# Performance work log

Hardware: AMD Instinct MI355X
Metric: run time of the kernel (lower is better)

Reference implementation:

```python
import jax, jax.numpy as jnp
import numpy as np

DIM = 1024
HEADS = 16
DIM_HEAD = 64
INNER = HEADS * DIM_HEAD  # 1024
SCALE = DIM_HEAD ** -0.5


def setup_inputs() -> dict:
    key = jax.random.key(0)
    k0, k1, k2 = jax.random.split(key, 3)
    x = jax.random.normal(k0, (4, 2048, DIM), dtype=jnp.float32)
    ln_gamma = jnp.ones((DIM,), dtype=jnp.float32)
    ln_beta = jnp.zeros((DIM,), dtype=jnp.float32)
    w_qkv = jax.random.normal(k1, (DIM, 3 * INNER), dtype=jnp.float32) * (DIM ** -0.5)
    w_out = jax.random.normal(k2, (INNER, DIM), dtype=jnp.float32) * (INNER ** -0.5)
    b_out = jnp.zeros((DIM,), dtype=jnp.float32)
    return {"x": x, "ln_gamma": ln_gamma, "ln_beta": ln_beta,
            "w_qkv": w_qkv, "w_out": w_out, "b_out": b_out}


def reference(x, ln_gamma, ln_beta, w_qkv, w_out, b_out):
    # LayerNorm over last dim (eps matches torch default 1e-5)
    mu = jnp.mean(x, axis=-1, keepdims=True)
    var = jnp.mean(jnp.square(x - mu), axis=-1, keepdims=True)
    xn = (x - mu) * jax.lax.rsqrt(var + 1e-5) * ln_gamma + ln_beta
    # QKV projection (no bias)
    qkv = xn @ w_qkv  # [b, t, 3*inner]
    q, k, v = jnp.split(qkv, 3, axis=-1)
    B, T, _ = x.shape
    def to_heads(t):
        return t.reshape(B, T, HEADS, DIM_HEAD).transpose(0, 2, 1, 3)  # b h t d
    q, k, v = to_heads(q), to_heads(k), to_heads(v)
    dots = jnp.einsum('bhid,bhjd->bhij', q, k) * SCALE
    attn = jax.nn.softmax(dots, axis=-1)
    out = jnp.einsum('bhij,bhjd->bhid', attn, v)
    out = out.transpose(0, 2, 1, 3).reshape(B, T, INNER)
    return out @ w_out + b_out
```

## Files before the change

### kernel.cpp

```cpp
#include <hip/hip_runtime.h>


#define DIMX 1024
#define TSEQ 2048
#define NB 4
#define NH 16
#define DH 64
#define NROWS (NB * TSEQ)
#define QSCALE 0.18033688011112042f

typedef __bf16 bf16_t;
typedef __bf16 bf16x8 __attribute__((ext_vector_type(8)));
typedef __bf16 bf16x4 __attribute__((ext_vector_type(4)));
typedef float f32x4 __attribute__((ext_vector_type(4)));

#if __has_builtin(__builtin_amdgcn_exp2f)
#define EXP2F __builtin_amdgcn_exp2f
#else
#define EXP2F exp2f
#endif

__device__ __forceinline__ bf16x4 cvt4(f32x4 v) {
    return __builtin_convertvector(v, bf16x4);
}
__device__ __forceinline__ void async16(const bf16_t* g, bf16_t* l) {
    __builtin_amdgcn_global_load_lds(
        (const __attribute__((address_space(1))) unsigned int*)g,
        (__attribute__((address_space(3))) unsigned int*)l, 16, 0, 0);
}

__global__ __launch_bounds__(256) void prep_kernel(
    const float* __restrict__ x, const float* __restrict__ g,
    const float* __restrict__ b, bf16_t* __restrict__ xn,
    const float* __restrict__ w_qkv, bf16_t* __restrict__ wqkvT,
    const float* __restrict__ w_out, bf16_t* __restrict__ woutT) {
    int bid = blockIdx.x, tid = threadIdx.x;
    if (bid < NROWS) {
        int row = bid;
        const float4 xv = *(const float4*)(x + (size_t)row * DIMX + tid * 4);
        float s = xv.x + xv.y + xv.z + xv.w;
        float q = xv.x * xv.x + xv.y * xv.y + xv.z * xv.z + xv.w * xv.w;
        for (int o = 32; o > 0; o >>= 1) {
            s += __shfl_xor(s, o);
            q += __shfl_xor(q, o);
        }
        __shared__ float2 red[4];
        int wave = tid >> 6, lane = tid & 63;
        if (lane == 0) red[wave] = make_float2(s, q);
        __syncthreads();
        float2 r0 = red[0], r1 = red[1], r2 = red[2], r3 = red[3];
        s = r0.x + r1.x + r2.x + r3.x;
        q = r0.y + r1.y + r2.y + r3.y;
        float mu = s * (1.0f / DIMX);
        float var = q * (1.0f / DIMX) - mu * mu;
        float rstd = rsqrtf(var + 1e-5f);
        float4 gv = *(const float4*)(g + tid * 4);
        float4 bv = *(const float4*)(b + tid * 4);
        f32x4 r;
        r[0] = (xv.x - mu) * rstd * gv.x + bv.x;
        r[1] = (xv.y - mu) * rstd * gv.y + bv.y;
        r[2] = (xv.z - mu) * rstd * gv.z + bv.z;
        r[3] = (xv.w - mu) * rstd * gv.w + bv.w;
        *(bf16x4*)(xn + (size_t)row * DIMX + tid * 4) = cvt4(r);
    } else {
        const float* src;
        bf16_t* dst;
        int R, C, tb;
        if (bid < NROWS + 3072) {
            tb = bid - NROWS; src = w_qkv; dst = wqkvT; R = 1024; C = 3072;
        } else {
            tb = bid - NROWS - 3072; src = w_out; dst = woutT; R = 1024; C = 1024;
        }
        int ntx = C >> 5;
        int c0 = (tb % ntx) * 32, r0 = (tb / ntx) * 32;
        int tx = tid & 31, ty = tid >> 5;
        __shared__ float tile[32][33];
        for (int i = ty; i < 32; i += 8)
            tile[i][tx] = src[(size_t)(r0 + i) * C + c0 + tx];
        __syncthreads();
        for (int i = ty; i < 32; i += 8)
            dst[(size_t)(c0 + i) * R + r0 + tx] = (bf16_t)tile[tx][i];
    }
}

#define MFMA16 __builtin_amdgcn_mfma_f32_16x16x32_bf16

template <int MODE>
__global__ __launch_bounds__(256, 2) void gemm128p(
    const bf16_t* __restrict__ A, const bf16_t* __restrict__ BT,
    void* __restrict__ Cout, const float* __restrict__ bias, int M, int N, int K) {
    __shared__ __align__(16) bf16_t As[2][128 * 64];
    __shared__ __align__(16) bf16_t Bs[2][128 * 64];
    int tid = threadIdx.x, lane = tid & 63, wave = tid >> 6;
    int lm = lane & 15, quad = lane >> 4;
    int wr = wave >> 1, wc = wave & 1;

    int nbx = gridDim.x;
    int nwg = nbx * gridDim.y;
    int linear = blockIdx.y * nbx + blockIdx.x;
    int cpx = nwg >> 3;
    int swz = (linear & 7) * cpx + (linear >> 3);
    int bx = swz % nbx, by = swz / nbx;
    int m0 = by * 128, n0 = bx * 128;

    int srow = tid >> 3, sc8 = tid & 7;
    int scol = (sc8 ^ (srow & 7)) << 3;
    const bf16_t* ga = A + (size_t)(m0 + srow) * K + scol;
    const bf16_t* gb = BT + (size_t)(n0 + srow) * K + scol;
    int ldst = tid << 3;

    int sw0 = ((quad ^ (lm & 7)) << 3);
    int sw1 = (((4 + quad) ^ (lm & 7)) << 3);

    f32x4 zero = {0.f, 0.f, 0.f, 0.f};
    f32x4 acc[4][4];
#pragma unroll
    for (int i = 0; i < 4; ++i)
#pragma unroll
        for (int j = 0; j < 4; ++j) acc[i][j] = zero;

#pragma unroll
    for (int i = 0; i < 4; ++i) async16(ga + (size_t)(i * 32) * K, &As[0][i * 2048 + ldst]);
#pragma unroll
    for (int i = 0; i < 4; ++i) async16(gb + (size_t)(i * 32) * K, &Bs[0][i * 2048 + ldst]);
    asm volatile("s_waitcnt vmcnt(0)" ::: "memory");
    __builtin_amdgcn_s_barrier();

    int nkt = K >> 6;
    for (int kt = 0; kt < nkt; ++kt) {
        int c = kt & 1;
        int k1 = (kt + 1) << 6;
        bool pf = (kt + 1) < nkt;
        const bf16_t* pa = &As[c][0];
        const bf16_t* pb = &Bs[c][0];
        bf16_t* na = &As[c ^ 1][0];
        bf16_t* nb = &Bs[c ^ 1][0];
        bf16x8 af[4][2], bfr[4][2];

#pragma unroll
        for (int t = 0; t < 4; ++t) {
            int ro = (wr * 64 + t * 16 + lm) * 64;
            af[t][0] = *(const bf16x8*)&pa[ro + sw0];
            af[t][1] = *(const bf16x8*)&pa[ro + sw1];
        }
#pragma unroll
        for (int t = 0; t < 4; ++t) {
            int ro = (wc * 64 + t * 16 + lm) * 64;
            bfr[t][0] = *(const bf16x8*)&pb[ro + sw0];
            bfr[t][1] = *(const bf16x8*)&pb[ro + sw1];
        }
        if (pf) {
#pragma unroll
            for (int i = 0; i < 4; ++i)
                async16(ga + (size_t)(i * 32) * K + k1, &na[i * 2048 + ldst]);
#pragma unroll
            for (int i = 0; i < 4; ++i)
                async16(gb + (size_t)(i * 32) * K + k1, &nb[i * 2048 + ldst]);
        }
        asm volatile("s_waitcnt lgkmcnt(0)" ::: "memory");
        __builtin_amdgcn_s_setprio(1);
#pragma unroll
        for (int mt = 0; mt < 4; ++mt)
#pragma unroll
            for (int nt = 0; nt < 4; ++nt) {
                acc[mt][nt] = MFMA16(af[mt][0], bfr[nt][0], acc[mt][nt], 0, 0, 0);
                acc[mt][nt] = MFMA16(af[mt][1], bfr[nt][1], acc[mt][nt], 0, 0, 0);
            }
        __builtin_amdgcn_s_setprio(0);
        asm volatile("s_waitcnt vmcnt(0)" ::: "memory");
        __builtin_amdgcn_s_barrier();
    }

#pragma unroll
    for (int mt = 0; mt < 4; ++mt) {
#pragma unroll
        for (int nt = 0; nt < 4; ++nt) {
            int m = m0 + wr * 64 + mt * 16 + quad * 4;
            int n = n0 + wc * 64 + nt * 16 + lm;
            if (MODE == 1) {
                int sel = n >> 10, nn = n & 1023, h = nn >> 6, d = nn & 63;
                int b = m >> 11, t = m & 2047;
                if (sel == 2) {
                    *(bf16x4*)((bf16_t*)Cout + (size_t)2 * 8388608 +
                               ((size_t)((b * NH + h) * DH + d)) * TSEQ + t) = cvt4(acc[mt][nt]);
                } else {
                    f32x4 sv = acc[mt][nt] * (sel == 0 ? QSCALE : 1.0f);
                    bf16x4 c4 = cvt4(sv);
#pragma unroll
                    for (int r = 0; r < 4; ++r)
                        ((bf16_t*)Cout)[(size_t)sel * 8388608 +
                                        ((size_t)((b * NH + h) * TSEQ + t + r)) * DH + d] = c4[r];
                }
            } else {
                float bn = bias[n];
#pragma unroll
                for (int r = 0; r < 4; ++r)
                    ((float*)Cout)[(size_t)(m + r) * N + n] = acc[mt][nt][r] + bn;
            }
        }
    }
}

__global__ __launch_bounds__(512, 4) void attn_mfma(
    const bf16_t* __restrict__ qkv, bf16_t* __restrict__ o) {
    int bh = blockIdx.y;
    int qt = blockIdx.x;
    const bf16_t* qb = qkv + (size_t)bh * TSEQ * DH;
    const bf16_t* kb = qkv + (size_t)8388608 + (size_t)bh * TSEQ * DH;
    const bf16_t* vb = qkv + (size_t)16777216 + (size_t)bh * DH * TSEQ;
    int tid = threadIdx.x, wave = tid >> 6, lane = tid & 63;
    int lm = lane & 15, quad = lane >> 4, lx = lm & 7;

    __shared__ __align__(16) bf16_t Ks[2][2][64 * 64];
    __shared__ __align__(16) bf16_t Vt[2][2][64 * 64];

    int roff = tid >> 3;
    int fr = (roff & 3) | ((roff & 8) >> 1);
    int cperm = ((tid & 7) ^ fr) * 8;
    const bf16_t* kp = kb + (size_t)roff * DH + cperm;
    const bf16_t* vp = vb + (size_t)roff * TSEQ + cperm;
    int l0 = tid * 8;

    bf16x8 qf[2][2];
#pragma unroll
    for (int u = 0; u < 2; ++u)
#pragma unroll
        for (int ks = 0; ks < 2; ++ks)
            qf[u][ks] = *(const bf16x8*)(qb +
                (size_t)(qt * 256 + wave * 32 + u * 16 + lm) * DH + ks * 32 + quad * 8);

    f32x4 zero = {0.f, 0.f, 0.f, 0.f};
    f32x4 m16 = {-16.f, -16.f, -16.f, -16.f};
    f32x4 acc[2][4];
#pragma unroll
    for (int u = 0; u < 2; ++u)
#pragma unroll
        for (int dt = 0; dt < 4; ++dt) acc[u][dt] = zero;
    f32x4 l4[2] = {zero, zero};

    int qh = lm >> 2, rr = lm & 3;
    int krow0 = 8 * qh + rr;
    int krow1 = krow0 + 4;
    int krow2 = 32 + 8 * (qh ^ 2) + rr;
    int krow3 = krow2 + 4;
    int fo0 = (quad ^ lx) * 8;
    int fo1 = ((4 + quad) ^ lx) * 8;
    int fv = (lm & 3) | ((lm & 8) >> 1);
    int vo0 = (quad ^ fv) * 8;
    int vo1 = ((4 | (quad ^ 2)) ^ fv) * 8;

    async16(kp, &Ks[0][0][l0]);
    async16(kp + (size_t)64 * DH, &Ks[0][1][l0]);
    async16(vp, &Vt[0][0][l0]);
    async16(vp + 64, &Vt[0][1][l0]);
    kp += 128 * DH; vp += 128;
    asm volatile("s_waitcnt vmcnt(0)" ::: "memory");
    __builtin_amdgcn_s_barrier();

    for (int jt = 0; jt < TSEQ / 128; ++jt) {
        int c = jt & 1;
        if (jt + 1 < TSEQ / 128) {
            async16(kp, &Ks[c ^ 1][0][l0]);
            async16(kp + (size_t)64 * DH, &Ks[c ^ 1][1][l0]);
            async16(vp, &Vt[c ^ 1][0][l0]);
            async16(vp + 64, &Vt[c ^ 1][1][l0]);
            kp += 128 * DH; vp += 128;
        }

#pragma unroll
        for (int sub = 0; sub < 2; ++sub) {
            const bf16_t* Kc = &Ks[c][sub][0];
            const bf16_t* Vc = &Vt[c][sub][0];

            bf16x8 kf[4][2];
            kf[0][0] = *(const bf16x8*)&Kc[krow0 * 64 + fo0];
            kf[0][1] = *(const bf16x8*)&Kc[krow0 * 64 + fo1];
            kf[1][0] = *(const bf16x8*)&Kc[krow1 * 64 + fo0];
            kf[1][1] = *(const bf16x8*)&Kc[krow1 * 64 + fo1];
            kf[2][0] = *(const bf16x8*)&Kc[krow2 * 64 + fo0];
            kf[2][1] = *(const bf16x8*)&Kc[krow2 * 64 + fo1];
            kf[3][0] = *(const bf16x8*)&Kc[krow3 * 64 + fo0];
            kf[3][1] = *(const bf16x8*)&Kc[krow3 * 64 + fo1];

            bf16x8 pf[2][2];
#pragma unroll
            for (int u = 0; u < 2; ++u) {
                f32x4 s[4];
                __builtin_amdgcn_s_setprio(1);
#pragma unroll
                for (int nt = 0; nt < 4; ++nt) {
                    s[nt] = __builtin_amdgcn_mfma_f32_16x16x32_bf16(kf[nt][0], qf[u][0], m16, 0, 0, 0);
                    s[nt] = __builtin_amdgcn_mfma_f32_16x16x32_bf16(kf[nt][1], qf[u][1], s[nt], 0, 0, 0);
                }
                __builtin_amdgcn_s_setprio(0);
                f32x4 p[4];
#pragma unroll
                for (int nt = 0; nt < 4; ++nt) {
#pragma unroll
                    for (int e = 0; e < 4; ++e) p[nt][e] = EXP2F(s[nt][e]);
                    l4[u] += p[nt];
                }
                bf16x4 c0 = cvt4(p[0]), c1 = cvt4(p[1]), c2 = cvt4(p[2]), c3 = cvt4(p[3]);
                pf[u][0] = __builtin_shufflevector(c0, c1, 0, 1, 2, 3, 4, 5, 6, 7);
                pf[u][1] = __builtin_shufflevector(c2, c3, 0, 1, 2, 3, 4, 5, 6, 7);
            }

            __builtin_amdgcn_s_setprio(1);
#pragma unroll
            for (int dt = 0; dt < 4; ++dt) {
                bf16x8 vf0 = *(const bf16x8*)&Vc[(dt * 16 + lm) * 64 + vo0];
                bf16x8 vf1 = *(const bf16x8*)&Vc[(dt * 16 + lm) * 64 + vo1];
#pragma unroll
                for (int u = 0; u < 2; ++u) {
                    acc[u][dt] = __builtin_amdgcn_mfma_f32_16x16x32_bf16(vf0, pf[u][0], acc[u][dt], 0, 0, 0);
                    acc[u][dt] = __builtin_amdgcn_mfma_f32_16x16x32_bf16(vf1, pf[u][1], acc[u][dt], 0, 0, 0);
                }
            }
            __builtin_amdgcn_s_setprio(0);
        }

        asm volatile("s_waitcnt vmcnt(0)" ::: "memory");
        __builtin_amdgcn_s_barrier();
    }

    int b = bh >> 4, h = bh & 15;
#pragma unroll
    for (int u = 0; u < 2; ++u) {
        float l = (l4[u][0] + l4[u][1]) + (l4[u][2] + l4[u][3]);
        l += __shfl_xor(l, 16);
        l += __shfl_xor(l, 32);
        float rl = 1.0f / l;
        int t = qt * 256 + wave * 32 + u * 16 + lm;
#pragma unroll
        for (int dt = 0; dt < 4; ++dt) {
            f32x4 ov = acc[u][dt] * rl;
            *(bf16x4*)(o + ((size_t)(b * TSEQ + t)) * DIMX + h * DH + dt * 16 + quad * 4) = cvt4(ov);
        }
    }
}

extern "C" void kernel_launch(void* const* d_in, const int* in_sizes, int n_in,
                              void* d_out, int out_size, void* d_ws, size_t ws_size,
                              hipStream_t stream) {
    const float* x = (const float*)d_in[0];
    const float* g = (const float*)d_in[1];
    const float* be = (const float*)d_in[2];
    const float* w_qkv = (const float*)d_in[3];
    const float* w_out = (const float*)d_in[4];
    const float* b_out = (const float*)d_in[5];
    float* out = (float*)d_out;
    char* ws = (char*)d_ws;

    bf16_t* xn = (bf16_t*)(ws);
    bf16_t* wqkvT = (bf16_t*)(ws + 16777216);
    bf16_t* woutT = (bf16_t*)(ws + 23068672);
    bf16_t* qkv = (bf16_t*)(ws + 25165824);
    bf16_t* attno = (bf16_t*)(ws + 75497472);

    prep_kernel<<<NROWS + 3072 + 1024, 256, 0, stream>>>(
        x, g, be, xn, w_qkv, wqkvT, w_out, woutT);
    gemm128p<1><<<dim3(24, 64), 256, 0, stream>>>(xn, wqkvT, (void*)qkv, nullptr, NROWS, 3072, 1024);
    attn_mfma<<<dim3(8, 64), 512, 0, stream>>>(qkv, attno);
    gemm128p<2><<<dim3(8, 64), 256, 0, stream>>>(attno, woutT, (void*)out, b_out, NROWS, 1024, 1024);
}
```

Before: 261.9 us.

## Add BK=32 GEMM for QKV projection and split B-fragment loads in out-proj GEMM

Adds a new GEMM kernel, used for the QKV projection, with a 32-wide K tile. This halves shared memory per block so 4 blocks can be resident per CU instead of 2, aiming to hide latency through higher occupancy at the cost of twice as many barrier-synchronised k-iterations. The output-projection GEMM is restructured to load B fragments in two halves with extra barriers, cutting register pressure but adding synchronisation. The shared epilogue is factored into a helper function.

```diff
diff --git a/kernel.cpp b/kernel.cpp
--- a/kernel.cpp
+++ b/kernel.cpp
@@ -86,91 +86,9 @@
 #define MFMA16 __builtin_amdgcn_mfma_f32_16x16x32_bf16
 
 template <int MODE>
-__global__ __launch_bounds__(256, 2) void gemm128p(
-    const bf16_t* __restrict__ A, const bf16_t* __restrict__ BT,
-    void* __restrict__ Cout, const float* __restrict__ bias, int M, int N, int K) {
-    __shared__ __align__(16) bf16_t As[2][128 * 64];
-    __shared__ __align__(16) bf16_t Bs[2][128 * 64];
-    int tid = threadIdx.x, lane = tid & 63, wave = tid >> 6;
-    int lm = lane & 15, quad = lane >> 4;
-    int wr = wave >> 1, wc = wave & 1;
-
-    int nbx = gridDim.x;
-    int nwg = nbx * gridDim.y;
-    int linear = blockIdx.y * nbx + blockIdx.x;
-    int cpx = nwg >> 3;
-    int swz = (linear & 7) * cpx + (linear >> 3);
-    int bx = swz % nbx, by = swz / nbx;
-    int m0 = by * 128, n0 = bx * 128;
-
-    int srow = tid >> 3, sc8 = tid & 7;
-    int scol = (sc8 ^ (srow & 7)) << 3;
-    const bf16_t* ga = A + (size_t)(m0 + srow) * K + scol;
-    const bf16_t* gb = BT + (size_t)(n0 + srow) * K + scol;
-    int ldst = tid << 3;
-
-    int sw0 = ((quad ^ (lm & 7)) << 3);
-    int sw1 = (((4 + quad) ^ (lm & 7)) << 3);
-
-    f32x4 zero = {0.f, 0.f, 0.f, 0.f};
-    f32x4 acc[4][4];
-#pragma unroll
-    for (int i = 0; i < 4; ++i)
-#pragma unroll
-        for (int j = 0; j < 4; ++j) acc[i][j] = zero;
-
-#pragma unroll
-    for (int i = 0; i < 4; ++i) async16(ga + (size_t)(i * 32) * K, &As[0][i * 2048 + ldst]);
-#pragma unroll
-    for (int i = 0; i < 4; ++i) async16(gb + (size_t)(i * 32) * K, &Bs[0][i * 2048 + ldst]);
-    asm volatile("s_waitcnt vmcnt(0)" ::: "memory");
-    __builtin_amdgcn_s_barrier();
-
-    int nkt = K >> 6;
-    for (int kt = 0; kt < nkt; ++kt) {
-        int c = kt & 1;
-        int k1 = (kt + 1) << 6;
-        bool pf = (kt + 1) < nkt;
-        const bf16_t* pa = &As[c][0];
-        const bf16_t* pb = &Bs[c][0];
-        bf16_t* na = &As[c ^ 1][0];
-        bf16_t* nb = &Bs[c ^ 1][0];
-        bf16x8 af[4][2], bfr[4][2];
-
-#pragma unroll
-        for (int t = 0; t < 4; ++t) {
-            int ro = (wr * 64 + t * 16 + lm) * 64;
-            af[t][0] = *(const bf16x8*)&pa[ro + sw0];
-            af[t][1] = *(const bf16x8*)&pa[ro + sw1];
-        }
-#pragma unroll
-        for (int t = 0; t < 4; ++t) {
-            int ro = (wc * 64 + t * 16 + lm) * 64;
-            bfr[t][0] = *(const bf16x8*)&pb[ro + sw0];
-            bfr[t][1] = *(const bf16x8*)&pb[ro + sw1];
-        }
-        if (pf) {
-#pragma unroll
-            for (int i = 0; i < 4; ++i)
-                async16(ga + (size_t)(i * 32) * K + k1, &na[i * 2048 + ldst]);
-#pragma unroll
-            for (int i = 0; i < 4; ++i)
-                async16(gb + (size_t)(i * 32) * K + k1, &nb[i * 2048 + ldst]);
-        }
-        asm volatile("s_waitcnt lgkmcnt(0)" ::: "memory");
-        __builtin_amdgcn_s_setprio(1);
-#pragma unroll
-        for (int mt = 0; mt < 4; ++mt)
-#pragma unroll
-            for (int nt = 0; nt < 4; ++nt) {
-                acc[mt][nt] = MFMA16(af[mt][0], bfr[nt][0], acc[mt][nt], 0, 0, 0);
-                acc[mt][nt] = MFMA16(af[mt][1], bfr[nt][1], acc[mt][nt], 0, 0, 0);
-            }
-        __builtin_amdgcn_s_setprio(0);
-        asm volatile("s_waitcnt vmcnt(0)" ::: "memory");
-        __builtin_amdgcn_s_barrier();
-    }
-
+__device__ __forceinline__ void gemm_epilogue(
+    f32x4 (&acc)[4][4], void* Cout, const float* bias,
+    int m0, int n0, int wr, int wc, int lm, int quad, int N) {
 #pragma unroll
     for (int mt = 0; mt < 4; ++mt) {
 #pragma unroll
@@ -201,6 +119,192 @@
     }
 }
 
+template <int MODE>
+__global__ __launch_bounds__(256, 4) void gemm128s(
+    const bf16_t* __restrict__ A, const bf16_t* __restrict__ BT,
+    void* __restrict__ Cout, const float* __restrict__ bias, int M, int N, int K) {
+    __shared__ __align__(16) bf16_t As[2][128 * 32];
+    __shared__ __align__(16) bf16_t Bs[2][128 * 32];
+    int tid = threadIdx.x, lane = tid & 63, wave = tid >> 6;
+    int lm = lane & 15, quad = lane >> 4;
+    int wr = wave >> 1, wc = wave & 1;
+
+    int nbx = gridDim.x;
+    int nwg = nbx * gridDim.y;
+    int linear = blockIdx.y * nbx + blockIdx.x;
+    int cpx = nwg >> 3;
+    int swz = (linear & 7) * cpx + (linear >> 3);
+    int bx = swz % nbx, by = swz / nbx;
+    int m0 = by * 128, n0 = bx * 128;
+
+    int srow = tid >> 2;
+    int scol = ((tid & 3) ^ ((tid >> 3) & 3)) << 3;
+    const bf16_t* ga = A + (size_t)(m0 + srow) * K + scol;
+    const bf16_t* gb = BT + (size_t)(n0 + srow) * K + scol;
+    int ldst = tid * 8;
+
+    int swr = ((quad ^ ((lm >> 1) & 3)) << 3);
+
+    f32x4 zero = {0.f, 0.f, 0.f, 0.f};
+    f32x4 acc[4][4];
+#pragma unroll
+    for (int i = 0; i < 4; ++i)
+#pragma unroll
+        for (int j = 0; j < 4; ++j) acc[i][j] = zero;
+
+    async16(ga, &As[0][ldst]);
+    async16(ga + (size_t)64 * K, &As[0][2048 + ldst]);
+    async16(gb, &Bs[0][ldst]);
+    async16(gb + (size_t)64 * K, &Bs[0][2048 + ldst]);
+    asm volatile("s_waitcnt vmcnt(0)" ::: "memory");
+    __builtin_amdgcn_s_barrier();
+
+    int nkt = K >> 5;
+    for (int kt = 0; kt < nkt; ++kt) {
+        int c = kt & 1;
+        int k1 = (kt + 1) << 5;
+        bool pf = (kt + 1) < nkt;
+        const bf16_t* pa = &As[c][0];
+        const bf16_t* pb = &Bs[c][0];
+        bf16_t* na = &As[c ^ 1][0];
+        bf16_t* nb = &Bs[c ^ 1][0];
+        bf16x8 af[4], bfr[4];
+#pragma unroll
+        for (int t = 0; t < 4; ++t)
+            af[t] = *(const bf16x8*)&pa[(wr * 64 + t * 16 + lm) * 32 + swr];
+#pragma unroll
+        for (int t = 0; t < 4; ++t)
+            bfr[t] = *(const bf16x8*)&pb[(wc * 64 + t * 16 + lm) * 32 + swr];
+        if (pf) {
+            async16(ga + k1, &na[ldst]);
+            async16(ga + (size_t)64 * K + k1, &na[2048 + ldst]);
+            async16(gb + k1, &nb[ldst]);
+            async16(gb + (size_t)64 * K + k1, &nb[2048 + ldst]);
+        }
+        asm volatile("s_waitcnt lgkmcnt(0)" ::: "memory");
+        __builtin_amdgcn_s_setprio(1);
+#pragma unroll
+        for (int mt = 0; mt < 4; ++mt)
+#pragma unroll
+            for (int nt = 0; nt < 4; ++nt)
+                acc[mt][nt] = MFMA16(af[mt], bfr[nt], acc[mt][nt], 0, 0, 0);
+        __builtin_amdgcn_s_setprio(0);
+        asm volatile("s_waitcnt vmcnt(0)" ::: "memory");
+        __builtin_amdgcn_s_barrier();
+    }
+
+    gemm_epilogue<MODE>(acc, Cout, bias, m0, n0, wr, wc, lm, quad, N);
+}
+
+template <int MODE>
+__global__ __launch_bounds__(256, 2) void gemm128p(
+    const bf16_t* __restrict__ A, const bf16_t* __restrict__ BT,
+    void* __restrict__ Cout, const float* __restrict__ bias, int M, int N, int K) {
+    __shared__ __align__(16) bf16_t As[2][128 * 64];
+    __shared__ __align__(16) bf16_t Bs[2][128 * 64];
+    int tid = threadIdx.x, lane = tid & 63, wave = tid >> 6;
+    int lm = lane & 15, quad = lane >> 4;
+    int wr = wave >> 1, wc = wave & 1;
+
+    int nbx = gridDim.x;
+    int nwg = nbx * gridDim.y;
+    int linear = blockIdx.y * nbx + blockIdx.x;
+    int cpx = nwg >> 3;
+    int swz = (linear & 7) * cpx + (linear >> 3);
+    int bx = swz % nbx, by = swz / nbx;
+    int m0 = by * 128, n0 = bx * 128;
+
+    int srow = tid >> 3, sc8 = tid & 7;
+    int scol = (sc8 ^ (srow & 7)) << 3;
+    const bf16_t* ga = A + (size_t)(m0 + srow) * K + scol;
+    const bf16_t* gb = BT + (size_t)(n0 + srow) * K + scol;
+    int ldst = tid << 3;
+
+    int sw0 = ((quad ^ (lm & 7)) << 3);
+    int sw1 = (((4 + quad) ^ (lm & 7)) << 3);
+
+    f32x4 zero = {0.f, 0.f, 0.f, 0.f};
+    f32x4 acc[4][4];
+#pragma unroll
+    for (int i = 0; i < 4; ++i)
+#pragma unroll
+        for (int j = 0; j < 4; ++j) acc[i][j] = zero;
+
+#pragma unroll
+    for (int i = 0; i < 4; ++i) async16(ga + (size_t)(i * 32) * K, &As[0][i * 2048 + ldst]);
+#pragma unroll
+    for (int i = 0; i < 4; ++i) async16(gb + (size_t)(i * 32) * K, &Bs[0][i * 2048 + ldst]);
+    asm volatile("s_waitcnt vmcnt(0)" ::: "memory");
+    __builtin_amdgcn_s_barrier();
+
+    int nkt = K >> 6;
+    for (int kt = 0; kt < nkt; ++kt) {
+        int c = kt & 1;
+        int k1 = (kt + 1) << 6;
+        bool pf = (kt + 1) < nkt;
+        const bf16_t* pa = &As[c][0];
+        const bf16_t* pb = &Bs[c][0];
+        bf16_t* na = &As[c ^ 1][0];
+        bf16_t* nb = &Bs[c ^ 1][0];
+        bf16x8 af[4][2], bfr[2][2];
+
+#pragma unroll
+        for (int t = 0; t < 4; ++t) {
+            int ro = (wr * 64 + t * 16 + lm) * 64;
+            af[t][0] = *(const bf16x8*)&pa[ro + sw0];
+            af[t][1] = *(const bf16x8*)&pa[ro + sw1];
+        }
+#pragma unroll
+        for (int t = 0; t < 2; ++t) {
+            int ro = (wc * 64 + t * 16 + lm) * 64;
+            bfr[t][0] = *(const bf16x8*)&pb[ro + sw0];
+            bfr[t][1] = *(const bf16x8*)&pb[ro + sw1];
+        }
+        if (pf) {
+#pragma unroll
+            for (int i = 0; i < 4; ++i)
+                async16(ga + (size_t)(i * 32) * K + k1, &na[i * 2048 + ldst]);
+#pragma unroll
+            for (int i = 0; i < 4; ++i)
+                async16(gb + (size_t)(i * 32) * K + k1, &nb[i * 2048 + ldst]);
+        }
+        __builtin_amdgcn_s_barrier();
+        asm volatile("s_waitcnt lgkmcnt(0)" ::: "memory");
+        __builtin_amdgcn_s_setprio(1);
+#pragma unroll
+        for (int mt = 0; mt < 4; ++mt)
+#pragma unroll
+            for (int nt = 0; nt < 2; ++nt) {
+                acc[mt][nt] = MFMA16(af[mt][0], bfr[nt][0], acc[mt][nt], 0, 0, 0);
+                acc[mt][nt] = MFMA16(af[mt][1], bfr[nt][1], acc[mt][nt], 0, 0, 0);
+            }
+        __builtin_amdgcn_s_setprio(0);
+        __builtin_amdgcn_s_barrier();
+
+#pragma unroll
+        for (int t = 0; t < 2; ++t) {
+            int ro = (wc * 64 + (2 + t) * 16 + lm) * 64;
+            bfr[t][0] = *(const bf16x8*)&pb[ro + sw0];
+            bfr[t][1] = *(const bf16x8*)&pb[ro + sw1];
+        }
+        __builtin_amdgcn_s_barrier();
+        asm volatile("s_waitcnt lgkmcnt(0)" ::: "memory");
+        __builtin_amdgcn_s_setprio(1);
+#pragma unroll
+        for (int mt = 0; mt < 4; ++mt)
+#pragma unroll
+            for (int nt = 0; nt < 2; ++nt) {
+                acc[mt][2 + nt] = MFMA16(af[mt][0], bfr[nt][0], acc[mt][2 + nt], 0, 0, 0);
+                acc[mt][2 + nt] = MFMA16(af[mt][1], bfr[nt][1], acc[mt][2 + nt], 0, 0, 0);
+            }
+        __builtin_amdgcn_s_setprio(0);
+        asm volatile("s_waitcnt vmcnt(0)" ::: "memory");
+        __builtin_amdgcn_s_barrier();
+    }
+
+    gemm_epilogue<MODE>(acc, Cout, bias, m0, n0, wr, wc, lm, quad, N);
+}
+
 __global__ __launch_bounds__(512, 4) void attn_mfma(
     const bf16_t* __restrict__ qkv, bf16_t* __restrict__ o) {
     int bh = blockIdx.y;
@@ -359,7 +463,7 @@
 
     prep_kernel<<<NROWS + 3072 + 1024, 256, 0, stream>>>(
         x, g, be, xn, w_qkv, wqkvT, w_out, woutT);
-    gemm128p<1><<<dim3(24, 64), 256, 0, stream>>>(xn, wqkvT, (void*)qkv, nullptr, NROWS, 3072, 1024);
+    gemm128s<1><<<dim3(24, 64), 256, 0, stream>>>(xn, wqkvT, (void*)qkv, nullptr, NROWS, 3072, 1024);
     attn_mfma<<<dim3(8, 64), 512, 0, stream>>>(qkv, attno);
     gemm128p<2><<<dim3(8, 64), 256, 0, stream>>>(attno, woutT, (void*)out, b_out, NROWS, 1024, 1024);
 }
```

After: 268.0 us. +2.3%, slower.

## Replace double-buffered GEMM with 4-stage K=32 async pipeline

Applied to the files above, without the earlier changes.

The GEMM kernel now uses a 4-deep ring of K=32 shared-memory tiles instead of two K=64 buffers. Three tiles are prefetched ahead, with partial vmcnt waits so global loads overlap several MFMA iterations. The goal is to hide global memory latency better at the same LDS footprint. In exchange, each barrier covers half as much MFMA work, so barriers and LDS read rounds double, and the swizzle pattern changes for the 32-wide rows.

```diff
diff --git a/kernel.cpp b/kernel.cpp
--- a/kernel.cpp
+++ b/kernel.cpp
@@ -86,91 +86,9 @@
 #define MFMA16 __builtin_amdgcn_mfma_f32_16x16x32_bf16
 
 template <int MODE>
-__global__ __launch_bounds__(256, 2) void gemm128p(
-    const bf16_t* __restrict__ A, const bf16_t* __restrict__ BT,
-    void* __restrict__ Cout, const float* __restrict__ bias, int M, int N, int K) {
-    __shared__ __align__(16) bf16_t As[2][128 * 64];
-    __shared__ __align__(16) bf16_t Bs[2][128 * 64];
-    int tid = threadIdx.x, lane = tid & 63, wave = tid >> 6;
-    int lm = lane & 15, quad = lane >> 4;
-    int wr = wave >> 1, wc = wave & 1;
-
-    int nbx = gridDim.x;
-    int nwg = nbx * gridDim.y;
-    int linear = blockIdx.y * nbx + blockIdx.x;
-    int cpx = nwg >> 3;
-    int swz = (linear & 7) * cpx + (linear >> 3);
-    int bx = swz % nbx, by = swz / nbx;
-    int m0 = by * 128, n0 = bx * 128;
-
-    int srow = tid >> 3, sc8 = tid & 7;
-    int scol = (sc8 ^ (srow & 7)) << 3;
-    const bf16_t* ga = A + (size_t)(m0 + srow) * K + scol;
-    const bf16_t* gb = BT + (size_t)(n0 + srow) * K + scol;
-    int ldst = tid << 3;
-
-    int sw0 = ((quad ^ (lm & 7)) << 3);
-    int sw1 = (((4 + quad) ^ (lm & 7)) << 3);
-
-    f32x4 zero = {0.f, 0.f, 0.f, 0.f};
-    f32x4 acc[4][4];
-#pragma unroll
-    for (int i = 0; i < 4; ++i)
-#pragma unroll
-        for (int j = 0; j < 4; ++j) acc[i][j] = zero;
-
-#pragma unroll
-    for (int i = 0; i < 4; ++i) async16(ga + (size_t)(i * 32) * K, &As[0][i * 2048 + ldst]);
-#pragma unroll
-    for (int i = 0; i < 4; ++i) async16(gb + (size_t)(i * 32) * K, &Bs[0][i * 2048 + ldst]);
-    asm volatile("s_waitcnt vmcnt(0)" ::: "memory");
-    __builtin_amdgcn_s_barrier();
-
-    int nkt = K >> 6;
-    for (int kt = 0; kt < nkt; ++kt) {
-        int c = kt & 1;
-        int k1 = (kt + 1) << 6;
-        bool pf = (kt + 1) < nkt;
-        const bf16_t* pa = &As[c][0];
-        const bf16_t* pb = &Bs[c][0];
-        bf16_t* na = &As[c ^ 1][0];
-        bf16_t* nb = &Bs[c ^ 1][0];
-        bf16x8 af[4][2], bfr[4][2];
-
-#pragma unroll
-        for (int t = 0; t < 4; ++t) {
-            int ro = (wr * 64 + t * 16 + lm) * 64;
-            af[t][0] = *(const bf16x8*)&pa[ro + sw0];
-            af[t][1] = *(const bf16x8*)&pa[ro + sw1];
-        }
-#pragma unroll
-        for (int t = 0; t < 4; ++t) {
-            int ro = (wc * 64 + t * 16 + lm) * 64;
-            bfr[t][0] = *(const bf16x8*)&pb[ro + sw0];
-            bfr[t][1] = *(const bf16x8*)&pb[ro + sw1];
-        }
-        if (pf) {
-#pragma unroll
-            for (int i = 0; i < 4; ++i)
-                async16(ga + (size_t)(i * 32) * K + k1, &na[i * 2048 + ldst]);
-#pragma unroll
-            for (int i = 0; i < 4; ++i)
-                async16(gb + (size_t)(i * 32) * K + k1, &nb[i * 2048 + ldst]);
-        }
-        asm volatile("s_waitcnt lgkmcnt(0)" ::: "memory");
-        __builtin_amdgcn_s_setprio(1);
-#pragma unroll
-        for (int mt = 0; mt < 4; ++mt)
-#pragma unroll
-            for (int nt = 0; nt < 4; ++nt) {
-                acc[mt][nt] = MFMA16(af[mt][0], bfr[nt][0], acc[mt][nt], 0, 0, 0);
-                acc[mt][nt] = MFMA16(af[mt][1], bfr[nt][1], acc[mt][nt], 0, 0, 0);
-            }
-        __builtin_amdgcn_s_setprio(0);
-        asm volatile("s_waitcnt vmcnt(0)" ::: "memory");
-        __builtin_amdgcn_s_barrier();
-    }
-
+__device__ __forceinline__ void gemm_epilogue(
+    f32x4 (&acc)[4][4], void* Cout, const float* bias,
+    int m0, int n0, int wr, int wc, int lm, int quad, int N) {
 #pragma unroll
     for (int mt = 0; mt < 4; ++mt) {
 #pragma unroll
@@ -201,6 +119,95 @@
     }
 }
 
+template <int MODE>
+__global__ __launch_bounds__(256, 2) void gemm128c(
+    const bf16_t* __restrict__ A, const bf16_t* __restrict__ BT,
+    void* __restrict__ Cout, const float* __restrict__ bias, int M, int N, int K) {
+    __shared__ __align__(16) bf16_t As[4][128 * 32];
+    __shared__ __align__(16) bf16_t Bs[4][128 * 32];
+    int tid = threadIdx.x, lane = tid & 63, wave = tid >> 6;
+    int lm = lane & 15, quad = lane >> 4;
+    int wr = wave >> 1, wc = wave & 1;
+
+    int nbx = gridDim.x;
+    int nwg = nbx * gridDim.y;
+    int linear = blockIdx.y * nbx + blockIdx.x;
+    int cpx = nwg >> 3;
+    int swz = (linear & 7) * cpx + (linear >> 3);
+    int bx = swz % nbx, by = swz / nbx;
+    int m0 = by * 128, n0 = bx * 128;
+
+    int srow = tid >> 2;
+    int scol = ((tid & 3) ^ ((tid >> 3) & 3)) << 3;
+    const bf16_t* ga = A + (size_t)(m0 + srow) * K + scol;
+    const bf16_t* gb = BT + (size_t)(n0 + srow) * K + scol;
+    int ldst = tid * 8;
+
+    int swr = ((quad ^ ((lm >> 1) & 3)) << 3);
+
+    f32x4 zero = {0.f, 0.f, 0.f, 0.f};
+    f32x4 acc[4][4];
+#pragma unroll
+    for (int i = 0; i < 4; ++i)
+#pragma unroll
+        for (int j = 0; j < 4; ++j) acc[i][j] = zero;
+
+#define STAGE_TILE(buf, kk)                                                   \
+    do {                                                                      \
+        async16(ga + (kk), &As[buf][ldst]);                                   \
+        async16(ga + (size_t)64 * K + (kk), &As[buf][2048 + ldst]);           \
+        async16(gb + (kk), &Bs[buf][ldst]);                                   \
+        async16(gb + (size_t)64 * K + (kk), &Bs[buf][2048 + ldst]);           \
+    } while (0)
+
+#define GEMM_BODY(buf)                                                        \
+    do {                                                                      \
+        const bf16_t* pa = &As[buf][0];                                       \
+        const bf16_t* pb = &Bs[buf][0];                                       \
+        bf16x8 af[4], bfr[4];                                                 \
+        _Pragma("unroll")                                                     \
+        for (int t = 0; t < 4; ++t)                                           \
+            af[t] = *(const bf16x8*)&pa[(wr * 64 + t * 16 + lm) * 32 + swr];  \
+        _Pragma("unroll")                                                     \
+        for (int t = 0; t < 4; ++t)                                           \
+            bfr[t] = *(const bf16x8*)&pb[(wc * 64 + t * 16 + lm) * 32 + swr]; \
+        asm volatile("s_waitcnt lgkmcnt(0)" ::: "memory");                    \
+        __builtin_amdgcn_s_setprio(1);                                        \
+        _Pragma("unroll")                                                     \
+        for (int mt = 0; mt < 4; ++mt)                                        \
+            _Pragma("unroll")                                                 \
+            for (int nt = 0; nt < 4; ++nt)                                    \
+                acc[mt][nt] = MFMA16(af[mt], bfr[nt], acc[mt][nt], 0, 0, 0);  \
+        __builtin_amdgcn_s_setprio(0);                                        \
+    } while (0)
+
+    STAGE_TILE(0, 0);
+    STAGE_TILE(1, 32);
+    STAGE_TILE(2, 64);
+    asm volatile("s_waitcnt vmcnt(8)" ::: "memory");
+    __builtin_amdgcn_s_barrier();
+
+    int nkt = K >> 5;
+    for (int kt = 0; kt + 3 < nkt; ++kt) {
+        STAGE_TILE((kt + 3) & 3, (size_t)(kt + 3) * 32);
+        GEMM_BODY(kt & 3);
+        asm volatile("s_waitcnt vmcnt(8)" ::: "memory");
+        __builtin_amdgcn_s_barrier();
+    }
+    GEMM_BODY((nkt - 3) & 3);
+    asm volatile("s_waitcnt vmcnt(4)" ::: "memory");
+    __builtin_amdgcn_s_barrier();
+    GEMM_BODY((nkt - 2) & 3);
+    asm volatile("s_waitcnt vmcnt(0)" ::: "memory");
+    __builtin_amdgcn_s_barrier();
+    GEMM_BODY((nkt - 1) & 3);
+
+#undef STAGE_TILE
+#undef GEMM_BODY
+
+    gemm_epilogue<MODE>(acc, Cout, bias, m0, n0, wr, wc, lm, quad, N);
+}
+
 __global__ __launch_bounds__(512, 4) void attn_mfma(
     const bf16_t* __restrict__ qkv, bf16_t* __restrict__ o) {
     int bh = blockIdx.y;
@@ -359,7 +366,7 @@
 
     prep_kernel<<<NROWS + 3072 + 1024, 256, 0, stream>>>(
         x, g, be, xn, w_qkv, wqkvT, w_out, woutT);
-    gemm128p<1><<<dim3(24, 64), 256, 0, stream>>>(xn, wqkvT, (void*)qkv, nullptr, NROWS, 3072, 1024);
+    gemm128c<1><<<dim3(24, 64), 256, 0, stream>>>(xn, wqkvT, (void*)qkv, nullptr, NROWS, 3072, 1024);
     attn_mfma<<<dim3(8, 64), 512, 0, stream>>>(qkv, attno);
-    gemm128p<2><<<dim3(8, 64), 256, 0, stream>>>(attno, woutT, (void*)out, b_out, NROWS, 1024, 1024);
-}
+    gemm128c<2><<<dim3(8, 64), 256, 0, stream>>>(attno, woutT, (void*)out, b_out, NROWS, 1024, 1024);
+}
```

Result: slower. 273.5 us (+4.4%).

## Split GEMM k-step into two barrier-separated halves and batch attention QK MFMAs

Applied to the files above, without the earlier changes.

The GEMM inner loop now loads only half of the B fragments, runs MFMAs on them, then loads the other half and runs the rest. Extra s_barrier calls separate the phases, apparently to keep waves in lockstep so LDS reads interleave with MFMA work, and fewer B registers are live at once. In attention, the QK^T MFMAs for both query sub-tiles are issued back to back before the exp2 softmax work, giving longer MFMA chains and more room to overlap. The trade-off is more barriers per k-step in the GEMM and more live score registers in attention.

```diff
diff --git a/kernel.cpp b/kernel.cpp
--- a/kernel.cpp
+++ b/kernel.cpp
@@ -86,91 +86,9 @@
 #define MFMA16 __builtin_amdgcn_mfma_f32_16x16x32_bf16
 
 template <int MODE>
-__global__ __launch_bounds__(256, 2) void gemm128p(
-    const bf16_t* __restrict__ A, const bf16_t* __restrict__ BT,
-    void* __restrict__ Cout, const float* __restrict__ bias, int M, int N, int K) {
-    __shared__ __align__(16) bf16_t As[2][128 * 64];
-    __shared__ __align__(16) bf16_t Bs[2][128 * 64];
-    int tid = threadIdx.x, lane = tid & 63, wave = tid >> 6;
-    int lm = lane & 15, quad = lane >> 4;
-    int wr = wave >> 1, wc = wave & 1;
-
-    int nbx = gridDim.x;
-    int nwg = nbx * gridDim.y;
-    int linear = blockIdx.y * nbx + blockIdx.x;
-    int cpx = nwg >> 3;
-    int swz = (linear & 7) * cpx + (linear >> 3);
-    int bx = swz % nbx, by = swz / nbx;
-    int m0 = by * 128, n0 = bx * 128;
-
-    int srow = tid >> 3, sc8 = tid & 7;
-    int scol = (sc8 ^ (srow & 7)) << 3;
-    const bf16_t* ga = A + (size_t)(m0 + srow) * K + scol;
-    const bf16_t* gb = BT + (size_t)(n0 + srow) * K + scol;
-    int ldst = tid << 3;
-
-    int sw0 = ((quad ^ (lm & 7)) << 3);
-    int sw1 = (((4 + quad) ^ (lm & 7)) << 3);
-
-    f32x4 zero = {0.f, 0.f, 0.f, 0.f};
-    f32x4 acc[4][4];
-#pragma unroll
-    for (int i = 0; i < 4; ++i)
-#pragma unroll
-        for (int j = 0; j < 4; ++j) acc[i][j] = zero;
-
-#pragma unroll
-    for (int i = 0; i < 4; ++i) async16(ga + (size_t)(i * 32) * K, &As[0][i * 2048 + ldst]);
-#pragma unroll
-    for (int i = 0; i < 4; ++i) async16(gb + (size_t)(i * 32) * K, &Bs[0][i * 2048 + ldst]);
-    asm volatile("s_waitcnt vmcnt(0)" ::: "memory");
-    __builtin_amdgcn_s_barrier();
-
-    int nkt = K >> 6;
-    for (int kt = 0; kt < nkt; ++kt) {
-        int c = kt & 1;
-        int k1 = (kt + 1) << 6;
-        bool pf = (kt + 1) < nkt;
-        const bf16_t* pa = &As[c][0];
-        const bf16_t* pb = &Bs[c][0];
-        bf16_t* na = &As[c ^ 1][0];
-        bf16_t* nb = &Bs[c ^ 1][0];
-        bf16x8 af[4][2], bfr[4][2];
-
-#pragma unroll
-        for (int t = 0; t < 4; ++t) {
-            int ro = (wr * 64 + t * 16 + lm) * 64;
-            af[t][0] = *(const bf16x8*)&pa[ro + sw0];
-            af[t][1] = *(const bf16x8*)&pa[ro + sw1];
-        }
-#pragma unroll
-        for (int t = 0; t < 4; ++t) {
-            int ro = (wc * 64 + t * 16 + lm) * 64;
-            bfr[t][0] = *(const bf16x8*)&pb[ro + sw0];
-            bfr[t][1] = *(const bf16x8*)&pb[ro + sw1];
-        }
-        if (pf) {
-#pragma unroll
-            for (int i = 0; i < 4; ++i)
-                async16(ga + (size_t)(i * 32) * K + k1, &na[i * 2048 + ldst]);
-#pragma unroll
-            for (int i = 0; i < 4; ++i)
-                async16(gb + (size_t)(i * 32) * K + k1, &nb[i * 2048 + ldst]);
-        }
-        asm volatile("s_waitcnt lgkmcnt(0)" ::: "memory");
-        __builtin_amdgcn_s_setprio(1);
-#pragma unroll
-        for (int mt = 0; mt < 4; ++mt)
-#pragma unroll
-            for (int nt = 0; nt < 4; ++nt) {
-                acc[mt][nt] = MFMA16(af[mt][0], bfr[nt][0], acc[mt][nt], 0, 0, 0);
-                acc[mt][nt] = MFMA16(af[mt][1], bfr[nt][1], acc[mt][nt], 0, 0, 0);
-            }
-        __builtin_amdgcn_s_setprio(0);
-        asm volatile("s_waitcnt vmcnt(0)" ::: "memory");
-        __builtin_amdgcn_s_barrier();
-    }
-
+__device__ __forceinline__ void gemm_epilogue(
+    f32x4 (&acc)[4][4], void* Cout, const float* bias,
+    int m0, int n0, int wr, int wc, int lm, int quad, int N) {
 #pragma unroll
     for (int mt = 0; mt < 4; ++mt) {
 #pragma unroll
@@ -201,6 +119,115 @@
     }
 }
 
+template <int MODE>
+__global__ __launch_bounds__(256, 2) void gemm128p(
+    const bf16_t* __restrict__ A, const bf16_t* __restrict__ BT,
+    void* __restrict__ Cout, const float* __restrict__ bias, int M, int N, int K) {
+    __shared__ __align__(16) bf16_t As[2][128 * 64];
+    __shared__ __align__(16) bf16_t Bs[2][128 * 64];
+    int tid = threadIdx.x, lane = tid & 63, wave = tid >> 6;
+    int lm = lane & 15, quad = lane >> 4;
+    int wr = wave >> 1, wc = wave & 1;
+
+    int nbx = gridDim.x;
+    int nwg = nbx * gridDim.y;
+    int linear = blockIdx.y * nbx + blockIdx.x;
+    int cpx = nwg >> 3;
+    int swz = (linear & 7) * cpx + (linear >> 3);
+    int bx = swz % nbx, by = swz / nbx;
+    int m0 = by * 128, n0 = bx * 128;
+
+    int srow = tid >> 3, sc8 = tid & 7;
+    int scol = (sc8 ^ (srow & 7)) << 3;
+    const bf16_t* ga = A + (size_t)(m0 + srow) * K + scol;
+    const bf16_t* gb = BT + (size_t)(n0 + srow) * K + scol;
+    int ldst = tid << 3;
+
+    int sw0 = ((quad ^ (lm & 7)) << 3);
+    int sw1 = (((4 + quad) ^ (lm & 7)) << 3);
+
+    f32x4 zero = {0.f, 0.f, 0.f, 0.f};
+    f32x4 acc[4][4];
+#pragma unroll
+    for (int i = 0; i < 4; ++i)
+#pragma unroll
+        for (int j = 0; j < 4; ++j) acc[i][j] = zero;
+
+#pragma unroll
+    for (int i = 0; i < 4; ++i) async16(ga + (size_t)(i * 32) * K, &As[0][i * 2048 + ldst]);
+#pragma unroll
+    for (int i = 0; i < 4; ++i) async16(gb + (size_t)(i * 32) * K, &Bs[0][i * 2048 + ldst]);
+    asm volatile("s_waitcnt vmcnt(0)" ::: "memory");
+    __builtin_amdgcn_s_barrier();
+
+    int nkt = K >> 6;
+    for (int kt = 0; kt < nkt; ++kt) {
+        int c = kt & 1;
+        int k1 = (kt + 1) << 6;
+        bool pf = (kt + 1) < nkt;
+        const bf16_t* pa = &As[c][0];
+        const bf16_t* pb = &Bs[c][0];
+        bf16_t* na = &As[c ^ 1][0];
+        bf16_t* nb = &Bs[c ^ 1][0];
+        bf16x8 af[4][2], bfr[2][2];
+
+#pragma unroll
+        for (int t = 0; t < 4; ++t) {
+            int ro = (wr * 64 + t * 16 + lm) * 64;
+            af[t][0] = *(const bf16x8*)&pa[ro + sw0];
+            af[t][1] = *(const bf16x8*)&pa[ro + sw1];
+        }
+#pragma unroll
+        for (int t = 0; t < 2; ++t) {
+            int ro = (wc * 64 + t * 16 + lm) * 64;
+            bfr[t][0] = *(const bf16x8*)&pb[ro + sw0];
+            bfr[t][1] = *(const bf16x8*)&pb[ro + sw1];
+        }
+        if (pf) {
+#pragma unroll
+            for (int i = 0; i < 4; ++i)
+                async16(ga + (size_t)(i * 32) * K + k1, &na[i * 2048 + ldst]);
+#pragma unroll
+            for (int i = 0; i < 4; ++i)
+                async16(gb + (size_t)(i * 32) * K + k1, &nb[i * 2048 + ldst]);
+        }
+        __builtin_amdgcn_s_barrier();
+        asm volatile("s_waitcnt lgkmcnt(0)" ::: "memory");
+        __builtin_amdgcn_s_setprio(1);
+#pragma unroll
+        for (int mt = 0; mt < 4; ++mt)
+#pragma unroll
+            for (int nt = 0; nt < 2; ++nt) {
+                acc[mt][nt] = MFMA16(af[mt][0], bfr[nt][0], acc[mt][nt], 0, 0, 0);
+                acc[mt][nt] = MFMA16(af[mt][1], bfr[nt][1], acc[mt][nt], 0, 0, 0);
+            }
+        __builtin_amdgcn_s_setprio(0);
+        __builtin_amdgcn_s_barrier();
+
+#pragma unroll
+        for (int t = 0; t < 2; ++t) {
+            int ro = (wc * 64 + (2 + t) * 16 + lm) * 64;
+            bfr[t][0] = *(const bf16x8*)&pb[ro + sw0];
+            bfr[t][1] = *(const bf16x8*)&pb[ro + sw1];
+        }
+        __builtin_amdgcn_s_barrier();
+        asm volatile("s_waitcnt lgkmcnt(0)" ::: "memory");
+        __builtin_amdgcn_s_setprio(1);
+#pragma unroll
+        for (int mt = 0; mt < 4; ++mt)
+#pragma unroll
+            for (int nt = 0; nt < 2; ++nt) {
+                acc[mt][2 + nt] = MFMA16(af[mt][0], bfr[nt][0], acc[mt][2 + nt], 0, 0, 0);
+                acc[mt][2 + nt] = MFMA16(af[mt][1], bfr[nt][1], acc[mt][2 + nt], 0, 0, 0);
+            }
+        __builtin_amdgcn_s_setprio(0);
+        asm volatile("s_waitcnt vmcnt(0)" ::: "memory");
+        __builtin_amdgcn_s_barrier();
+    }
+
+    gemm_epilogue<MODE>(acc, Cout, bias, m0, n0, wr, wc, lm, quad, N);
+}
+
 __global__ __launch_bounds__(512, 4) void attn_mfma(
     const bf16_t* __restrict__ qkv, bf16_t* __restrict__ o) {
     int bh = blockIdx.y;
@@ -282,22 +309,25 @@
             kf[3][0] = *(const bf16x8*)&Kc[krow3 * 64 + fo0];
             kf[3][1] = *(const bf16x8*)&Kc[krow3 * 64 + fo1];
 
+            f32x4 s2[2][4];
+            __builtin_amdgcn_s_setprio(1);
+#pragma unroll
+            for (int u = 0; u < 2; ++u)
+#pragma unroll
+                for (int nt = 0; nt < 4; ++nt) {
+                    s2[u][nt] = __builtin_amdgcn_mfma_f32_16x16x32_bf16(kf[nt][0], qf[u][0], m16, 0, 0, 0);
+                    s2[u][nt] = __builtin_amdgcn_mfma_f32_16x16x32_bf16(kf[nt][1], qf[u][1], s2[u][nt], 0, 0, 0);
+                }
+            __builtin_amdgcn_s_setprio(0);
+
             bf16x8 pf[2][2];
 #pragma unroll
             for (int u = 0; u < 2; ++u) {
-                f32x4 s[4];
-                __builtin_amdgcn_s_setprio(1);
+                f32x4 p[4];
 #pragma unroll
                 for (int nt = 0; nt < 4; ++nt) {
-                    s[nt] = __builtin_amdgcn_mfma_f32_16x16x32_bf16(kf[nt][0], qf[u][0], m16, 0, 0, 0);
-                    s[nt] = __builtin_amdgcn_mfma_f32_16x16x32_bf16(kf[nt][1], qf[u][1], s[nt], 0, 0, 0);
-                }
-                __builtin_amdgcn_s_setprio(0);
-                f32x4 p[4];
-#pragma unroll
-                for (int nt = 0; nt < 4; ++nt) {
-#pragma unroll
-                    for (int e = 0; e < 4; ++e) p[nt][e] = EXP2F(s[nt][e]);
+#pragma unroll
+                    for (int e = 0; e < 4; ++e) p[nt][e] = EXP2F(s2[u][nt][e]);
                     l4[u] += p[nt];
                 }
                 bf16x4 c0 = cvt4(p[0]), c1 = cvt4(p[1]), c2 = cvt4(p[2]), c3 = cvt4(p[3]);
```

After: 258.4 us (median of 2 runs). Within noise of the previous version (-1.3%).
